# Kernel tuning notes

Hardware: AMD Instinct MI355X
Metric: run time of the kernel (lower is better)

## Reference

```python
import jax, jax.numpy as jnp
import numpy as np
from jax.ops import segment_sum

N_NODES = 100000


def _deg_inv_sqrt(idx, n):
    # DGL GraphConv norm='both': degs clamped to min 1, then deg^{-0.5}
    deg = segment_sum(jnp.ones_like(idx, dtype=jnp.float32), idx, num_segments=n)
    return jnp.where(deg > 0, jax.lax.rsqrt(jnp.maximum(deg, 1.0)), 1.0)


def _graph_conv(x, src, dst, W, b, out_norm, in_norm, n):
    # norm='both': scale src feats by out_deg^-1/2, sum-aggregate, scale by in_deg^-1/2
    h = (x * out_norm[:, None]) @ W          # apply weight first (cheaper/equal width)
    msg = h[src]                              # [E, d] irregular gather
    agg = segment_sum(msg, dst, num_segments=n)
    return agg * in_norm[:, None] + b


def setup_inputs() -> dict:
    key = jax.random.key(0)
    k1, k2, k3, k4, k5, k6, k7 = jax.random.split(key, 7)
    E = 1600000
    in_feats, h_feats, out_feats = 128, 128, 64
    in_feat = jax.random.normal(k1, (N_NODES, in_feats), dtype=jnp.float32)
    src = jax.random.randint(k2, (E,), 0, N_NODES, dtype=jnp.int32)
    dst = jax.random.randint(k3, (E,), 0, N_NODES, dtype=jnp.int32)
    # Glorot-style init like dgl GraphConv
    W1 = jax.random.normal(k4, (in_feats, h_feats), dtype=jnp.float32) * (1.0 / np.sqrt(in_feats))
    b1 = jnp.zeros((h_feats,), dtype=jnp.float32)
    W2 = jax.random.normal(k5, (h_feats, out_feats), dtype=jnp.float32) * (1.0 / np.sqrt(h_feats))
    b2 = jnp.zeros((out_feats,), dtype=jnp.float32)
    return {"in_feat": in_feat, "src": src, "dst": dst, "W1": W1, "b1": b1, "W2": W2, "b2": b2}


def reference(in_feat, src, dst, W1, b1, W2, b2):
    n = in_feat.shape[0]
    out_norm = _deg_inv_sqrt(src, n)  # out-degree norm (source side)
    in_norm = _deg_inv_sqrt(dst, n)   # in-degree norm (destination side)
    h = _graph_conv(in_feat, src, dst, W1, b1, out_norm, in_norm, n)
    z = jax.nn.relu(h)
    h2 = _graph_conv(z, src, dst, W2, b2, out_norm, in_norm, n)
    return (h2, z)
```

## Files before the change

kernel.cpp:

```cpp
#include <hip/hip_runtime.h>

#define N_NODES 100000
#define N_EDGES 1600000
#define NB 391
#define BCAP 5120
#define PART_BLOCKS 250
#define EPB 6400

typedef __attribute__((ext_vector_type(8))) short short8;
typedef __attribute__((ext_vector_type(4))) float f32x4;

__device__ inline unsigned short f2bf(float f) {
    unsigned int u = __builtin_bit_cast(unsigned int, f);
    u += 0x7fffu + ((u >> 16) & 1u);
    return (unsigned short)(u >> 16);
}
__device__ inline float bf2f(unsigned short h) {
    unsigned int u = ((unsigned int)h) << 16;
    return __builtin_bit_cast(float, u);
}

__global__ __launch_bounds__(256) void k_part(const int* __restrict__ src, const int* __restrict__ dst,
                                              int* __restrict__ gcurD, int* __restrict__ gcurS,
                                              unsigned int* __restrict__ ebuf,
                                              unsigned char* __restrict__ ebufS,
                                              const float* __restrict__ W1, const float* __restrict__ W2,
                                              unsigned short* __restrict__ Wp1, unsigned short* __restrict__ Wp2) {
    if (blockIdx.x >= PART_BLOCKS) {
        int i = (blockIdx.x - PART_BLOCKS) * 256 + threadIdx.x;
        if (i < 2048) {
            int kq = i >> 7, c = i & 127;
#pragma unroll
            for (int j = 0; j < 8; j++) Wp1[i * 8 + j] = f2bf(W1[(kq * 8 + j) * 128 + c]);
        } else if (i < 3072) {
            int i2 = i - 2048;
            int kq = i2 >> 6, c = i2 & 63;
#pragma unroll
            for (int j = 0; j < 8; j++) Wp2[i2 * 8 + j] = f2bf(W2[(kq * 8 + j) * 64 + c]);
        }
        return;
    }
    __shared__ int histD[NB], gbaseD[NB];
    __shared__ int histS[NB], gbaseS[NB];
    for (int i = threadIdx.x; i < NB; i += 256) { histD[i] = 0; histS[i] = 0; }
    __syncthreads();
    int base = blockIdx.x * EPB;
    for (int i = threadIdx.x; i < EPB; i += 256) {
        int d = dst[base + i], s = src[base + i];
        atomicAdd(&histD[d >> 8], 1);
        atomicAdd(&histS[s >> 8], 1);
    }
    __syncthreads();
    for (int i = threadIdx.x; i < NB; i += 256) {
        gbaseD[i] = atomicAdd(&gcurD[i], histD[i]);
        gbaseS[i] = atomicAdd(&gcurS[i], histS[i]);
        histD[i] = 0;
        histS[i] = 0;
    }
    __syncthreads();
    for (int i = threadIdx.x; i < EPB; i += 256) {
        int d = dst[base + i], s = src[base + i];
        int bd = d >> 8;
        int r = atomicAdd(&histD[bd], 1);
        int pos = gbaseD[bd] + r;
        if (pos < BCAP) ebuf[(size_t)bd * BCAP + pos] = ((unsigned int)s << 8) | (unsigned int)(d & 255);
        int bs = s >> 8;
        int r2 = atomicAdd(&histS[bs], 1);
        int pos2 = gbaseS[bs] + r2;
        if (pos2 < BCAP) ebufS[(size_t)bs * BCAP + pos2] = (unsigned char)(s & 255);
    }
}

__global__ __launch_bounds__(256) void k_bhist_scan(const unsigned char* __restrict__ ebufS,
                                                    const int* __restrict__ gcurS,
                                                    float* __restrict__ out_norm,
                                                    const int* __restrict__ gcurD,
                                                    int* __restrict__ bbase, int* __restrict__ row_ptr) {
    int t = threadIdx.x;
    if (blockIdx.x < NB) {
        __shared__ int hist[256];
        int b = blockIdx.x;
        hist[t] = 0;
        __syncthreads();
        int ne = min(gcurS[b], BCAP);
        const unsigned char* eb = ebufS + (size_t)b * BCAP;
        for (int i = t; i < ne; i += 256) atomicAdd(&hist[eb[i]], 1);
        __syncthreads();
        int node = b * 256 + t;
        if (node < N_NODES) out_norm[node] = hist[t] > 0 ? rsqrtf((float)hist[t]) : 1.0f;
    } else {
        __shared__ int s[NB + 1];
        for (int i = t; i < NB; i += 256) s[i] = min(gcurD[i], BCAP);
        __syncthreads();
        if (t == 0) {
            int run = 0;
            for (int b = 0; b < NB; b++) { int v = s[b]; s[b] = run; run += v; }
            s[NB] = run;
        }
        __syncthreads();
        for (int i = t; i < NB + 1; i += 256) bbase[i] = s[i];
        if (t == 0) row_ptr[N_NODES] = s[NB];
    }
}

__global__ __launch_bounds__(256) void k_bsort_xb(const unsigned int* __restrict__ ebuf, const int* __restrict__ gcurD,
                                                  const int* __restrict__ bbase, int* __restrict__ csr_src,
                                                  int* __restrict__ row_ptr, float* __restrict__ in_norm,
                                                  const float* __restrict__ x, const float* __restrict__ out_norm,
                                                  unsigned short* __restrict__ xb) {
    __shared__ unsigned int st[BCAP];
    __shared__ int perm[BCAP];
    __shared__ int hist[256], cursor[256], sa[256], sb[256];
    int t = threadIdx.x;
    if (blockIdx.x >= NB) {
        int tid = (blockIdx.x - NB) * 256 + t;
        int row = tid >> 5;
        float4 v = ((const float4*)x)[tid];
        float w = out_norm[row];
        unsigned int lo = (unsigned int)f2bf(v.x * w) | ((unsigned int)f2bf(v.y * w) << 16);
        unsigned int hi = (unsigned int)f2bf(v.z * w) | ((unsigned int)f2bf(v.w * w) << 16);
        ((uint2*)xb)[tid] = make_uint2(lo, hi);
        return;
    }
    int b = blockIdx.x;
    int ne = min(gcurD[b], BCAP);
    const unsigned int* eb = ebuf + (size_t)b * BCAP;
    hist[t] = 0;
    __syncthreads();
    for (int i = t; i < ne; i += 256) {
        unsigned int pk = eb[i];
        st[i] = pk;
        atomicAdd(&hist[pk & 255u], 1);
    }
    __syncthreads();
    sa[t] = hist[t];
    __syncthreads();
    int* cur = sa; int* nxt = sb;
    for (int o = 1; o < 256; o <<= 1) {
        int v = cur[t] + (t >= o ? cur[t - o] : 0);
        nxt[t] = v;
        __syncthreads();
        int* tmp = cur; cur = nxt; nxt = tmp;
    }
    int ex = cur[t] - hist[t];
    cursor[t] = ex;
    int node = b * 256 + t;
    if (node < N_NODES) {
        row_ptr[node] = bbase[b] + ex;
        in_norm[node] = hist[t] > 0 ? rsqrtf((float)hist[t]) : 1.0f;
    }
    __syncthreads();
    for (int i = t; i < ne; i += 256) {
        unsigned int pk = st[i];
        int pos = atomicAdd(&cursor[pk & 255u], 1);
        perm[pos] = (int)(pk >> 8);
    }
    __syncthreads();
    int gb = bbase[b];
    for (int i = t; i < ne; i += 256) csr_src[gb + i] = perm[i];
}

__global__ __launch_bounds__(256) void k_agg1(const unsigned short* __restrict__ xb,
                                              const int* __restrict__ row_ptr, const int* __restrict__ csr,
                                              const float* __restrict__ in_norm,
                                              unsigned short* __restrict__ aggb) {
    int wave = threadIdx.x >> 6, lane = threadIdx.x & 63;
    int d = blockIdx.x * 4 + wave;
    if (d >= N_NODES) return;
    int e0 = __builtin_amdgcn_readfirstlane(row_ptr[d]);
    int e1 = __builtin_amdgcn_readfirstlane(row_ptr[d + 1]);
    int col = lane << 1;
    float accL[8], accH[8];
#pragma unroll
    for (int j = 0; j < 8; j++) { accL[j] = 0.f; accH[j] = 0.f; }
    int e = e0;
    for (; e + 8 <= e1; e += 8) {
        int sI[8];
#pragma unroll
        for (int j = 0; j < 8; j++) sI[j] = __builtin_amdgcn_readfirstlane(csr[e + j]);
        unsigned int v[8];
#pragma unroll
        for (int j = 0; j < 8; j++) v[j] = *(const unsigned int*)(xb + (size_t)sI[j] * 128 + col);
#pragma unroll
        for (int j = 0; j < 8; j++) {
            accL[j] += bf2f((unsigned short)(v[j] & 0xffffu));
            accH[j] += bf2f((unsigned short)(v[j] >> 16));
        }
    }
    for (; e < e1; e++) {
        int s = __builtin_amdgcn_readfirstlane(csr[e]);
        unsigned int v = *(const unsigned int*)(xb + (size_t)s * 128 + col);
        accL[0] += bf2f((unsigned short)(v & 0xffffu));
        accH[0] += bf2f((unsigned short)(v >> 16));
    }
    float a0 = 0.f, a1 = 0.f;
#pragma unroll
    for (int j = 0; j < 8; j++) { a0 += accL[j]; a1 += accH[j]; }
    float w = in_norm[d];
    unsigned int pk = (unsigned int)f2bf(a0 * w) | ((unsigned int)f2bf(a1 * w) << 16);
    *(unsigned int*)(aggb + (size_t)d * 128 + col) = pk;
}

__global__ __launch_bounds__(256) void k_gemm12(const unsigned short* __restrict__ Ab,
                                                const unsigned short* __restrict__ Wp1,
                                                const unsigned short* __restrict__ Wp2,
                                                const float* __restrict__ bias1,
                                                const float* __restrict__ out_norm,
                                                float* __restrict__ z_out,
                                                unsigned short* __restrict__ tb) {
    __shared__ __align__(16) unsigned short lds1[16 * 128 * 8];
    __shared__ __align__(16) unsigned short lds2[16 * 64 * 8];
    __shared__ __align__(16) unsigned short zt[64 * 132];
    {
        const uint4* s1 = (const uint4*)Wp1; uint4* d1 = (uint4*)lds1;
        for (int i = threadIdx.x; i < 2048; i += 256) d1[i] = s1[i];
        const uint4* s2 = (const uint4*)Wp2; uint4* d2 = (uint4*)lds2;
        for (int i = threadIdx.x; i < 1024; i += 256) d2[i] = s2[i];
    }
    __syncthreads();
    int wave = threadIdx.x >> 6, lane = threadIdx.x & 63;
    int base = (blockIdx.x * 4 + wave) * 16;
    if (base >= N_NODES) return;
    int m = lane & 15, q = lane >> 4;
    short8 a[4];
#pragma unroll
    for (int t = 0; t < 4; t++) a[t] = *(const short8*)(Ab + (size_t)(base + m) * 128 + t * 32 + q * 8);
    f32x4 acc[8];
#pragma unroll
    for (int c = 0; c < 8; c++) acc[c] = (f32x4)(0.f);
#pragma unroll
    for (int ct = 0; ct < 8; ct++) {
#pragma unroll
        for (int t = 0; t < 4; t++) {
            short8 b = *(const short8*)(lds1 + ((t * 4 + q) * 128 + ct * 16 + m) * 8);
            acc[ct] = __builtin_amdgcn_mfma_f32_16x16x32_bf16(a[t], b, acc[ct], 0, 0, 0);
        }
    }
    float onr[4];
#pragma unroll
    for (int i = 0; i < 4; i++) onr[i] = out_norm[base + q * 4 + i];
#pragma unroll
    for (int ct = 0; ct < 8; ct++) {
        int col = ct * 16 + m;
        float bv = bias1[col];
#pragma unroll
        for (int i = 0; i < 4; i++) {
            int row = base + q * 4 + i;
            float v = acc[ct][i] + bv;
            v = v > 0.f ? v : 0.f;
            z_out[(size_t)row * 128 + col] = v;
            zt[(wave * 16 + q * 4 + i) * 132 + col] = f2bf(v * onr[i]);
        }
    }
    short8 a2[4];
#pragma unroll
    for (int t = 0; t < 4; t++) a2[t] = *(const short8*)(zt + (wave * 16 + m) * 132 + t * 32 + q * 8);
    f32x4 acc2[4];
#pragma unroll
    for (int c = 0; c < 4; c++) acc2[c] = (f32x4)(0.f);
#pragma unroll
    for (int ct = 0; ct < 4; ct++) {
#pragma unroll
        for (int t = 0; t < 4; t++) {
            short8 b = *(const short8*)(lds2 + ((t * 4 + q) * 64 + ct * 16 + m) * 8);
            acc2[ct] = __builtin_amdgcn_mfma_f32_16x16x32_bf16(a2[t], b, acc2[ct], 0, 0, 0);
        }
    }
#pragma unroll
    for (int ct = 0; ct < 4; ct++) {
        int col = ct * 16 + m;
#pragma unroll
        for (int i = 0; i < 4; i++) {
            int row = base + q * 4 + i;
            tb[(size_t)row * 64 + col] = f2bf(acc2[ct][i]);
        }
    }
}

__global__ __launch_bounds__(256) void k_agg2(const unsigned short* __restrict__ tb,
                                              const int* __restrict__ row_ptr, const int* __restrict__ csr,
                                              const float* __restrict__ in_norm, const float* __restrict__ b2,
                                              float* __restrict__ out_h2) {
    int wave = threadIdx.x >> 6, lane = threadIdx.x & 63;
    int d = blockIdx.x * 4 + wave;
    if (d >= N_NODES) return;
    int e0 = __builtin_amdgcn_readfirstlane(row_ptr[d]);
    int e1 = __builtin_amdgcn_readfirstlane(row_ptr[d + 1]);
    float acc[8];
#pragma unroll
    for (int j = 0; j < 8; j++) acc[j] = 0.f;
    int e = e0;
    for (; e + 8 <= e1; e += 8) {
        int sI[8];
#pragma unroll
        for (int j = 0; j < 8; j++) sI[j] = __builtin_amdgcn_readfirstlane(csr[e + j]);
        unsigned short v[8];
#pragma unroll
        for (int j = 0; j < 8; j++) v[j] = tb[(size_t)sI[j] * 64 + lane];
#pragma unroll
        for (int j = 0; j < 8; j++) acc[j] += bf2f(v[j]);
    }
    for (; e < e1; e++) {
        int s = __builtin_amdgcn_readfirstlane(csr[e]);
        acc[0] += bf2f(tb[(size_t)s * 64 + lane]);
    }
    float a = 0.f;
#pragma unroll
    for (int j = 0; j < 8; j++) a += acc[j];
    out_h2[(size_t)d * 64 + lane] = a * in_norm[d] + b2[lane];
}

extern "C" void kernel_launch(void* const* d_in, const int* in_sizes, int n_in,
                              void* d_out, int out_size, void* d_ws, size_t ws_size,
                              hipStream_t stream) {
    const float* x   = (const float*)d_in[0];
    const int*   src = (const int*)d_in[1];
    const int*   dst = (const int*)d_in[2];
    const float* W1  = (const float*)d_in[3];
    const float* b1  = (const float*)d_in[4];
    const float* W2  = (const float*)d_in[5];
    const float* b2  = (const float*)d_in[6];
    float* out_h2 = (float*)d_out;
    float* out_z  = (float*)d_out + N_NODES * 64;

    char* ws = (char*)d_ws;
    size_t off = 0;
    auto alloc = [&](size_t bytes) -> char* {
        char* p = ws + off;
        off = (off + bytes + 255) & ~(size_t)255;
        return p;
    };
    int* gcurD    = (int*)alloc(NB * 4);
    int* gcurS    = (int*)alloc(NB * 4);
    int* bbase    = (int*)alloc((NB + 1) * 4);
    int* row_ptr  = (int*)alloc((N_NODES + 1) * 4);
    float* out_norm = (float*)alloc(N_NODES * 4);
    float* in_norm  = (float*)alloc(N_NODES * 4);
    unsigned int* ebuf = (unsigned int*)alloc((size_t)NB * BCAP * 4);
    unsigned char* ebufS = (unsigned char*)alloc((size_t)NB * BCAP);
    int* csr_src  = (int*)alloc((size_t)N_EDGES * 4);
    unsigned short* Wp1 = (unsigned short*)alloc(2048 * 8 * 2);
    unsigned short* Wp2 = (unsigned short*)alloc(1024 * 8 * 2);
    unsigned short* xb    = (unsigned short*)alloc((size_t)N_NODES * 128 * 2);
    unsigned short* agg1b = (unsigned short*)alloc((size_t)N_NODES * 128 * 2);
    unsigned short* tb    = (unsigned short*)alloc((size_t)N_NODES * 64 * 2);
    (void)ws_size; (void)in_sizes; (void)n_in; (void)out_size;

    hipMemsetAsync(gcurD, 0, NB * 4, stream);
    hipMemsetAsync(gcurS, 0, NB * 4, stream);

    const int GD_AGG = (N_NODES + 3) / 4;
    const int GD_GEMM = (N_NODES / 16 + 3) / 4;
    const int GD_XB = N_NODES * 32 / 256;

    k_part<<<PART_BLOCKS + 12, 256, 0, stream>>>(src, dst, gcurD, gcurS, ebuf, ebufS, W1, W2, Wp1, Wp2);
    k_bhist_scan<<<NB + 1, 256, 0, stream>>>(ebufS, gcurS, out_norm, gcurD, bbase, row_ptr);
    k_bsort_xb<<<NB + GD_XB, 256, 0, stream>>>(ebuf, gcurD, bbase, csr_src, row_ptr, in_norm, x, out_norm, xb);
    k_agg1<<<GD_AGG, 256, 0, stream>>>(xb, row_ptr, csr_src, in_norm, agg1b);
    k_gemm12<<<GD_GEMM, 256, 0, stream>>>(agg1b, Wp1, Wp2, b1, out_norm, out_z, tb);
    k_agg2<<<GD_AGG, 256, 0, stream>>>(tb, row_ptr, csr_src, in_norm, b2, out_h2);
}
```

Before: 317.8 us.

## Retune partition kernel, pad global counters, vectorize histogram, unroll aggregation tails

The partition kernel now runs more blocks with fewer edges each and caches src/dst in shared memory so the second pass does not reread global memory. Global bucket counters are padded to separate cache lines to reduce atomic contention, and zero-count atomics are skipped. The out-degree histogram reads bytes four at a time, the bucket sort rereads edges from global memory instead of staging them in shared memory, and the aggregation tail loops are unrolled into 4/2/1 steps. The result is less global traffic and contention, at the cost of more blocks and extra shared memory in the partition kernel.

```diff
diff --git a/kernel.cpp b/kernel.cpp
--- a/kernel.cpp
+++ b/kernel.cpp
@@ -4,8 +4,9 @@
 #define N_EDGES 1600000
 #define NB 391
 #define BCAP 5120
-#define PART_BLOCKS 250
-#define EPB 6400
+#define PART_BLOCKS 800
+#define EPB 2000
+#define GSTRIDE 16
 
 typedef __attribute__((ext_vector_type(8))) short short8;
 typedef __attribute__((ext_vector_type(4))) float f32x4;
@@ -42,24 +43,28 @@
     }
     __shared__ int histD[NB], gbaseD[NB];
     __shared__ int histS[NB], gbaseS[NB];
+    __shared__ uint2 est[EPB];
     for (int i = threadIdx.x; i < NB; i += 256) { histD[i] = 0; histS[i] = 0; }
     __syncthreads();
     int base = blockIdx.x * EPB;
     for (int i = threadIdx.x; i < EPB; i += 256) {
         int d = dst[base + i], s = src[base + i];
+        est[i] = make_uint2((unsigned int)s, (unsigned int)d);
         atomicAdd(&histD[d >> 8], 1);
         atomicAdd(&histS[s >> 8], 1);
     }
     __syncthreads();
     for (int i = threadIdx.x; i < NB; i += 256) {
-        gbaseD[i] = atomicAdd(&gcurD[i], histD[i]);
-        gbaseS[i] = atomicAdd(&gcurS[i], histS[i]);
+        int hD = histD[i], hS = histS[i];
+        gbaseD[i] = hD ? atomicAdd(&gcurD[i * GSTRIDE], hD) : 0;
+        gbaseS[i] = hS ? atomicAdd(&gcurS[i * GSTRIDE], hS) : 0;
         histD[i] = 0;
         histS[i] = 0;
     }
     __syncthreads();
     for (int i = threadIdx.x; i < EPB; i += 256) {
-        int d = dst[base + i], s = src[base + i];
+        uint2 e2 = est[i];
+        int s = (int)e2.x, d = (int)e2.y;
         int bd = d >> 8;
         int r = atomicAdd(&histD[bd], 1);
         int pos = gbaseD[bd] + r;
@@ -82,15 +87,22 @@
         int b = blockIdx.x;
         hist[t] = 0;
         __syncthreads();
-        int ne = min(gcurS[b], BCAP);
+        int ne = min(gcurS[b * GSTRIDE], BCAP);
         const unsigned char* eb = ebufS + (size_t)b * BCAP;
-        for (int i = t; i < ne; i += 256) atomicAdd(&hist[eb[i]], 1);
+        int nv = ne >> 2;
+        const uchar4* ev = (const uchar4*)eb;
+        for (int i = t; i < nv; i += 256) {
+            uchar4 u = ev[i];
+            atomicAdd(&hist[u.x], 1); atomicAdd(&hist[u.y], 1);
+            atomicAdd(&hist[u.z], 1); atomicAdd(&hist[u.w], 1);
+        }
+        for (int i = (nv << 2) + t; i < ne; i += 256) atomicAdd(&hist[eb[i]], 1);
         __syncthreads();
         int node = b * 256 + t;
         if (node < N_NODES) out_norm[node] = hist[t] > 0 ? rsqrtf((float)hist[t]) : 1.0f;
     } else {
         __shared__ int s[NB + 1];
-        for (int i = t; i < NB; i += 256) s[i] = min(gcurD[i], BCAP);
+        for (int i = t; i < NB; i += 256) s[i] = min(gcurD[i * GSTRIDE], BCAP);
         __syncthreads();
         if (t == 0) {
             int run = 0;
@@ -108,7 +120,6 @@
                                                   int* __restrict__ row_ptr, float* __restrict__ in_norm,
                                                   const float* __restrict__ x, const float* __restrict__ out_norm,
                                                   unsigned short* __restrict__ xb) {
-    __shared__ unsigned int st[BCAP];
     __shared__ int perm[BCAP];
     __shared__ int hist[256], cursor[256], sa[256], sb[256];
     int t = threadIdx.x;
@@ -123,15 +134,11 @@
         return;
     }
     int b = blockIdx.x;
-    int ne = min(gcurD[b], BCAP);
+    int ne = min(gcurD[b * GSTRIDE], BCAP);
     const unsigned int* eb = ebuf + (size_t)b * BCAP;
     hist[t] = 0;
     __syncthreads();
-    for (int i = t; i < ne; i += 256) {
-        unsigned int pk = eb[i];
-        st[i] = pk;
-        atomicAdd(&hist[pk & 255u], 1);
-    }
+    for (int i = t; i < ne; i += 256) atomicAdd(&hist[eb[i] & 255u], 1);
     __syncthreads();
     sa[t] = hist[t];
     __syncthreads();
@@ -151,7 +158,7 @@
     }
     __syncthreads();
     for (int i = t; i < ne; i += 256) {
-        unsigned int pk = st[i];
+        unsigned int pk = eb[i];
         int pos = atomicAdd(&cursor[pk & 255u], 1);
         perm[pos] = (int)(pk >> 8);
     }
@@ -187,7 +194,35 @@
             accH[j] += bf2f((unsigned short)(v[j] >> 16));
         }
     }
-    for (; e < e1; e++) {
+    if (e + 4 <= e1) {
+        int sI[4];
+#pragma unroll
+        for (int j = 0; j < 4; j++) sI[j] = __builtin_amdgcn_readfirstlane(csr[e + j]);
+        unsigned int v[4];
+#pragma unroll
+        for (int j = 0; j < 4; j++) v[j] = *(const unsigned int*)(xb + (size_t)sI[j] * 128 + col);
+#pragma unroll
+        for (int j = 0; j < 4; j++) {
+            accL[j] += bf2f((unsigned short)(v[j] & 0xffffu));
+            accH[j] += bf2f((unsigned short)(v[j] >> 16));
+        }
+        e += 4;
+    }
+    if (e + 2 <= e1) {
+        int sI[2];
+#pragma unroll
+        for (int j = 0; j < 2; j++) sI[j] = __builtin_amdgcn_readfirstlane(csr[e + j]);
+        unsigned int v[2];
+#pragma unroll
+        for (int j = 0; j < 2; j++) v[j] = *(const unsigned int*)(xb + (size_t)sI[j] * 128 + col);
+#pragma unroll
+        for (int j = 0; j < 2; j++) {
+            accL[j] += bf2f((unsigned short)(v[j] & 0xffffu));
+            accH[j] += bf2f((unsigned short)(v[j] >> 16));
+        }
+        e += 2;
+    }
+    if (e < e1) {
         int s = __builtin_amdgcn_readfirstlane(csr[e]);
         unsigned int v = *(const unsigned int*)(xb + (size_t)s * 128 + col);
         accL[0] += bf2f((unsigned short)(v & 0xffffu));
@@ -300,7 +335,29 @@
 #pragma unroll
         for (int j = 0; j < 8; j++) acc[j] += bf2f(v[j]);
     }
-    for (; e < e1; e++) {
+    if (e + 4 <= e1) {
+        int sI[4];
+#pragma unroll
+        for (int j = 0; j < 4; j++) sI[j] = __builtin_amdgcn_readfirstlane(csr[e + j]);
+        unsigned short v[4];
+#pragma unroll
+        for (int j = 0; j < 4; j++) v[j] = tb[(size_t)sI[j] * 64 + lane];
+#pragma unroll
+        for (int j = 0; j < 4; j++) acc[j] += bf2f(v[j]);
+        e += 4;
+    }
+    if (e + 2 <= e1) {
+        int sI[2];
+#pragma unroll
+        for (int j = 0; j < 2; j++) sI[j] = __builtin_amdgcn_readfirstlane(csr[e + j]);
+        unsigned short v[2];
+#pragma unroll
+        for (int j = 0; j < 2; j++) v[j] = tb[(size_t)sI[j] * 64 + lane];
+#pragma unroll
+        for (int j = 0; j < 2; j++) acc[j] += bf2f(v[j]);
+        e += 2;
+    }
+    if (e < e1) {
         int s = __builtin_amdgcn_readfirstlane(csr[e]);
         acc[0] += bf2f(tb[(size_t)s * 64 + lane]);
     }
@@ -330,8 +387,8 @@
         off = (off + bytes + 255) & ~(size_t)255;
         return p;
     };
-    int* gcurD    = (int*)alloc(NB * 4);
-    int* gcurS    = (int*)alloc(NB * 4);
+    int* gcurD    = (int*)alloc(NB * GSTRIDE * 4);
+    int* gcurS    = (int*)alloc(NB * GSTRIDE * 4);
     int* bbase    = (int*)alloc((NB + 1) * 4);
     int* row_ptr  = (int*)alloc((N_NODES + 1) * 4);
     float* out_norm = (float*)alloc(N_NODES * 4);
@@ -346,8 +403,8 @@
     unsigned short* tb    = (unsigned short*)alloc((size_t)N_NODES * 64 * 2);
     (void)ws_size; (void)in_sizes; (void)n_in; (void)out_size;
 
-    hipMemsetAsync(gcurD, 0, NB * 4, stream);
-    hipMemsetAsync(gcurS, 0, NB * 4, stream);
+    hipMemsetAsync(gcurD, 0, NB * GSTRIDE * 4, stream);
+    hipMemsetAsync(gcurS, 0, NB * GSTRIDE * 4, stream);
 
     const int GD_AGG = (N_NODES + 3) / 4;
     const int GD_GEMM = (N_NODES / 16 + 3) / 4;
```

Result: slower. 332.1 us (+4.5%).
